# Performance work log

Measured on AMD Instinct MI355X. Metric: run time of the kernel, lower is better.

The kernel has to match this reference:

```python
import jax, jax.numpy as jnp
import numpy as np
from jax import lax

NPOINT = 1024
RADIUS = 0.4
NSAMPLE = 32


def _fps(xyz, m):
    """Farthest point sampling. xyz: (B,N,3) -> idx (B,m) int32."""
    B, N, _ = xyz.shape
    init_idx = jnp.zeros((B,), jnp.int32)

    def step(carry, _):
        dists, last = carry  # dists (B,N), last (B,)
        last_pt = jnp.take_along_axis(xyz, last[:, None, None], axis=1)  # (B,1,3)
        d = jnp.sum((xyz - last_pt) ** 2, axis=-1)  # (B,N)
        dists = jnp.minimum(dists, d)
        nxt = jnp.argmax(dists, axis=-1).astype(jnp.int32)
        return (dists, nxt), nxt

    (_, _), rest = lax.scan(step, (jnp.full((B, N), 1e10, jnp.float32), init_idx),
                            None, length=m - 1)
    return jnp.concatenate([init_idx[None, :], rest], axis=0).T  # (B,m)


def _ball_query(xyz, new_xyz, radius, k):
    """First-k in-radius neighbors (CUDA ball_query semantics: pad with first hit).
    xyz (B,N,3), new_xyz (B,M,3) -> (B,M,k) int32."""
    N = xyz.shape[1]
    d2 = jnp.sum((new_xyz[:, :, None, :] - xyz[:, None, :, :]) ** 2, axis=-1)  # (B,M,N)
    idx = jnp.where(d2 < radius * radius, jnp.arange(N, dtype=jnp.int32), jnp.int32(N))
    neg_topk, _ = lax.top_k(-idx, k)        # k smallest indices
    idx_k = -neg_topk                        # (B,M,k), invalid == N
    valid = idx_k < N
    first = idx_k[..., :1]                   # first (closest-index) hit
    return jnp.where(valid, idx_k, first)


def _gather(pts, idx):
    """pts (B,N,D), idx (B,M,K) -> (B,M,K,D)."""
    return jax.vmap(lambda p, i: p[i])(pts, idx)


def setup_inputs() -> dict:
    key = jax.random.key(0)
    ks = jax.random.split(key, 6)
    B, N, C = 8, 8192, 64
    cin = C + 3
    xyz = jax.random.normal(ks[0], (B, N, 3), jnp.float32)
    features = jax.random.normal(ks[1], (B, N, C), jnp.float32)
    w1 = jax.random.normal(ks[2], (64, cin), jnp.float32) * 0.05
    b1 = jnp.zeros((64,), jnp.float32)
    w2 = jax.random.normal(ks[3], (64, 64), jnp.float32) * 0.05
    b2 = jnp.zeros((64,), jnp.float32)
    w3 = jax.random.normal(ks[4], (128, 64), jnp.float32) * 0.05
    b3 = jnp.zeros((128,), jnp.float32)
    return {"xyz": xyz, "features": features, "w1": w1, "b1": b1,
            "w2": w2, "b2": b2, "w3": w3, "b3": b3}


def reference(xyz, features, w1, b1, w2, b2, w3, b3):
    # FPS sample npoint centers (pool=True branch)
    fps_idx = _fps(xyz, NPOINT)                                   # (B,M)
    new_xyz = jnp.take_along_axis(xyz, fps_idx[..., None], axis=1)  # (B,M,3)
    # ball-query grouping with use_xyz=True (relative coords prepended)
    gidx = _ball_query(xyz, new_xyz, RADIUS, NSAMPLE)             # (B,M,K)
    gxyz = _gather(xyz, gidx) - new_xyz[:, :, None, :]            # (B,M,K,3)
    gfeat = _gather(features, gidx)                               # (B,M,K,C)
    x = jnp.concatenate([gxyz, gfeat], axis=-1)                   # (B,M,K,3+C)
    # shared MLP (1x1 convs) + ReLU
    h = jax.nn.relu(jnp.einsum('bmkc,oc->bmko', x, w1) + b1)
    h = jax.nn.relu(jnp.einsum('bmkc,oc->bmko', h, w2) + b2)
    h = jax.nn.relu(jnp.einsum('bmkc,oc->bmko', h, w3) + b3)      # (B,M,K,128)
    # max-pool over group dim -> (B, C_out, M) like torch (B, mlp[-1], npoint)
    new_features = jnp.transpose(jnp.max(h, axis=2), (0, 2, 1))
    return new_xyz, new_features
```

## Files before the change

### kernel.cpp

```cpp
#include <hip/hip_runtime.h>
#include <stdint.h>

#define BB 8
#define NN 8192
#define NPOINT 1024
#define NSAMPLE 32
#define XS 104
#define HS 72

typedef short short8 __attribute__((ext_vector_type(8)));
typedef float floatx4 __attribute__((ext_vector_type(4)));
typedef float f32x2 __attribute__((ext_vector_type(2)));

__device__ __forceinline__ unsigned short f2bf(float f) {
    unsigned u = __float_as_uint(f);
    unsigned r = u + 0x7FFFu + ((u >> 16) & 1u);
    return (unsigned short)(r >> 16);
}

__device__ __forceinline__ unsigned long long u64max(unsigned long long a,
                                                     unsigned long long b) {
    return (a > b) ? a : b;
}

template <int CTRL, int RMASK>
__device__ __forceinline__ unsigned long long dpp_max_step(unsigned long long key) {
    int lo = (int)(unsigned int)(key & 0xffffffffull);
    int hi = (int)(unsigned int)(key >> 32);
    int tlo = __builtin_amdgcn_update_dpp(0, lo, CTRL, RMASK, 0xF, true);
    int thi = __builtin_amdgcn_update_dpp(0, hi, CTRL, RMASK, 0xF, true);
    unsigned long long t = ((unsigned long long)(unsigned int)thi << 32) |
                           (unsigned long long)(unsigned int)tlo;
    return u64max(key, t);
}

__device__ __forceinline__ unsigned long long dpp_wave_max(unsigned long long key) {
    key = dpp_max_step<0x111, 0xF>(key);
    key = dpp_max_step<0x112, 0xF>(key);
    key = dpp_max_step<0x114, 0xF>(key);
    key = dpp_max_step<0x118, 0xF>(key);
    key = dpp_max_step<0x142, 0xA>(key);
    key = dpp_max_step<0x143, 0xC>(key);
    return key;
}

__device__ __forceinline__ void fps_bar() {
    asm volatile("s_waitcnt lgkmcnt(0)" ::: "memory");
    __builtin_amdgcn_s_barrier();
    asm volatile("" ::: "memory");
}

__global__ __launch_bounds__(256) void mega_kernel(
    const float* __restrict__ xyz, const float* __restrict__ features,
    const float* __restrict__ w1, const float* __restrict__ b1,
    const float* __restrict__ w2, const float* __restrict__ b2,
    const float* __restrict__ w3, const float* __restrict__ b3,
    float* __restrict__ new_xyz, float* __restrict__ out_feat,
    unsigned* __restrict__ sel) {
    __shared__ __align__(16) char smem[98432];

    const int t = threadIdx.x;
    const int lane = t & 63;

    if (blockIdx.x < BB) {
#pragma clang fp contract(off)
        const int b = blockIdx.x;
        float* sxyz = (float*)smem;
        unsigned long long* wred = (unsigned long long*)(smem + 98304);
        const int wv = t >> 6;
        const float* base = xyz + (size_t)b * NN * 3;
        unsigned* selb = sel + b * NPOINT;

        f32x2 px2[16], py2[16], pz2[16];
        float dist[32];
#pragma unroll
        for (int i = 0; i < 32; ++i) {
            int p = t + (i << 8);
            float x = base[p * 3 + 0];
            float y = base[p * 3 + 1];
            float z = base[p * 3 + 2];
            sxyz[p * 3 + 0] = x; sxyz[p * 3 + 1] = y; sxyz[p * 3 + 2] = z;
            if (i & 1) { px2[i >> 1].y = x; py2[i >> 1].y = y; pz2[i >> 1].y = z; }
            else       { px2[i >> 1].x = x; py2[i >> 1].x = y; pz2[i >> 1].x = z; }
            dist[i] = 1e10f;
        }
        __syncthreads();

        float lx = sxyz[0], ly = sxyz[1], lz = sxyz[2];
        float* outb = new_xyz + (size_t)b * NPOINT * 3;
        if (t == 0) {
            outb[0] = lx; outb[1] = ly; outb[2] = lz;
            __hip_atomic_store(&selb[0], 1u, __ATOMIC_RELAXED,
                               __HIP_MEMORY_SCOPE_AGENT);
        }

        for (int j = 1; j < NPOINT; ++j) {
            float bd0 = -1.0f, bd1 = -1.0f;
            int bi0 = 0, bi1 = 16;
            f32x2 lx2; lx2.x = lx; lx2.y = lx;
            f32x2 ly2; ly2.x = ly; ly2.y = ly;
            f32x2 lz2; lz2.x = lz; lz2.y = lz;
#pragma unroll
            for (int jj = 0; jj < 16; ++jj) {
                f32x2 dx = px2[jj] - lx2;
                f32x2 dy = py2[jj] - ly2;
                f32x2 dz = pz2[jj] - lz2;
                f32x2 xx = dx * dx;
                f32x2 yy = dy * dy;
                f32x2 zz = dz * dz;
                f32x2 s1 = xx + yy;
                f32x2 d2 = s1 + zz;
                float d0 = fminf(dist[2 * jj], d2.x);
                dist[2 * jj] = d0;
                float d1 = fminf(dist[2 * jj + 1], d2.y);
                dist[2 * jj + 1] = d1;
                bool ge = d0 >= d1;
                float pm = ge ? d0 : d1;
                int pi = ge ? (2 * jj) : (2 * jj + 1);
                if (jj < 8) {
                    bool gt = pm > bd0;
                    bd0 = gt ? pm : bd0;
                    bi0 = gt ? pi : bi0;
                } else {
                    bool gt = pm > bd1;
                    bd1 = gt ? pm : bd1;
                    bi1 = gt ? pi : bi1;
                }
            }
            unsigned long long key0 =
                ((unsigned long long)__float_as_uint(bd0) << 32) |
                (unsigned long long)(~(unsigned int)(t + (bi0 << 8)));
            unsigned long long key1 =
                ((unsigned long long)__float_as_uint(bd1) << 32) |
                (unsigned long long)(~(unsigned int)(t + (bi1 << 8)));
            unsigned long long key = u64max(key0, key1);
            key = dpp_wave_max(key);
            if (lane == 63) wred[(j & 1) * 4 + wv] = key;
            fps_bar();
            int cur;
            {
                const unsigned long long* wr = &wred[(j & 1) * 4];
                ulonglong2 p01 = *(const ulonglong2*)&wr[0];
                ulonglong2 p23 = *(const ulonglong2*)&wr[2];
                unsigned long long m = u64max(u64max(p01.x, p01.y),
                                              u64max(p23.x, p23.y));
                cur = (int)(~(unsigned int)(m & 0xffffffffull));
            }
            {
                const float* cp = &sxyz[cur * 3];
                float3 c = *(const float3*)cp;
                lx = c.x; ly = c.y; lz = c.z;
            }
            if (t == 0) {
                outb[j * 3 + 0] = lx;
                outb[j * 3 + 1] = ly;
                outb[j * 3 + 2] = lz;
                __hip_atomic_store(&selb[j], (unsigned)(cur + 1),
                                   __ATOMIC_RELAXED, __HIP_MEMORY_SCOPE_AGENT);
            }
        }
    } else {
        const int i = blockIdx.x - BB;
        const int b = i & 7;
        const int g = i >> 3;
        unsigned short* s_x = (unsigned short*)smem;
        unsigned short* s_h = (unsigned short*)(smem + 26624);
        unsigned short* s_w12 = (unsigned short*)(smem + 45056);
        int* s_gi = (int*)(smem + 67584);
        int* s_sel4 = (int*)(smem + 68096);

        const int w = t >> 6;
        const int col = lane & 15;
        const int quad = lane >> 4;

        {
            int o = t >> 2, part = t & 3;
            const float* w1r = w1 + o * 67;
#pragma unroll
            for (int ii = 0; ii < 26; ++ii) {
                int c = part * 26 + ii;
                float v = 0.0f;
                if (c < 64) v = w1r[3 + c];
                else if (c < 67) v = w1r[c - 64];
                s_w12[o * XS + c] = f2bf(v);
            }
            const float* w2r = w2 + o * 64 + part * 16;
#pragma unroll
            for (int ii = 0; ii < 8; ++ii) {
                unsigned pk = (unsigned)f2bf(w2r[2 * ii]) |
                              ((unsigned)f2bf(w2r[2 * ii + 1]) << 16);
                *(unsigned*)&s_w12[6656 + o * HS + part * 16 + 2 * ii] = pk;
            }
        }

        if (t < 4) {
            unsigned* sp = sel + b * NPOINT + (g << 2) + t;
            unsigned v;
            while ((( v = __hip_atomic_load(sp, __ATOMIC_RELAXED,
                                            __HIP_MEMORY_SCOPE_AGENT)) - 1u) > 8191u)
                __builtin_amdgcn_s_sleep(32);
            s_sel4[t] = (int)(v - 1u);
        }
        __syncthreads();

        {
            const int cidx = s_sel4[w];
            const float* base = xyz + (size_t)b * NN * 3;
            const float cx = base[cidx * 3 + 0];
            const float cy = base[cidx * 3 + 1];
            const float cz = base[cidx * 3 + 2];
            const float R2 = (float)(0.4 * 0.4);

            int have = 0;
            for (int chunk = 0; chunk < (NN / 64) && have < NSAMPLE; ++chunk) {
                int p = (chunk << 6) + lane;
                float dx = __fsub_rn(cx, base[p * 3 + 0]);
                float dy = __fsub_rn(cy, base[p * 3 + 1]);
                float dz = __fsub_rn(cz, base[p * 3 + 2]);
                float d2 = __fadd_rn(__fadd_rn(__fmul_rn(dx, dx), __fmul_rn(dy, dy)),
                                     __fmul_rn(dz, dz));
                bool in = d2 < R2;
                unsigned long long m = __ballot(in);
                int pre = __popcll(m & ((1ull << lane) - 1ull));
                int slot = have + pre;
                if (in && slot < NSAMPLE) s_gi[w * NSAMPLE + slot] = p;
                have += (int)__popcll(m);
            }
            if (lane < NSAMPLE) {
                int first = s_gi[w * NSAMPLE];
                int v = (lane < have) ? s_gi[w * NSAMPLE + lane] : first;
                s_gi[w * NSAMPLE + lane] = v;
            }
        }
        __syncthreads();

        {
            int k = t >> 1, half = t & 1;
            int row = s_gi[k];
            const float4* frow =
                (const float4*)(features + ((size_t)b * NN + row) * 64) + half * 8;
            unsigned short* xr = &s_x[k * XS + half * 32];
#pragma unroll
            for (int ii = 0; ii < 8; ++ii) {
                float4 v = frow[ii];
                unsigned lo = (unsigned)f2bf(v.x) | ((unsigned)f2bf(v.y) << 16);
                unsigned hi = (unsigned)f2bf(v.z) | ((unsigned)f2bf(v.w) << 16);
                *(uint2*)(xr + ii * 4) = make_uint2(lo, hi);
            }
        }
        if (t < 128) {
            int k = t;
            int row = s_gi[k];
            int cidx = s_sel4[k >> 5];
            const float* pr = xyz + ((size_t)b * NN + row) * 3;
            const float* cr = xyz + ((size_t)b * NN + cidx) * 3;
            s_x[k * XS + 64] = f2bf(pr[0] - cr[0]);
            s_x[k * XS + 65] = f2bf(pr[1] - cr[1]);
            s_x[k * XS + 66] = f2bf(pr[2] - cr[2]);
            s_x[k * XS + 67] = 0;
            unsigned* z = (unsigned*)&s_x[k * XS + 68];
#pragma unroll
            for (int ii = 0; ii < 14; ++ii) z[ii] = 0;
        }
        __syncthreads();

        const int mbase = w * 32;

        floatx4 acc[2][4] = {};
        for (int kk = 0; kk < 3; ++kk) {
            short8 a0 = *(const short8*)&s_x[(mbase + col) * XS + kk * 32 + quad * 8];
            short8 a1 = *(const short8*)&s_x[(mbase + 16 + col) * XS + kk * 32 + quad * 8];
#pragma unroll
            for (int nt = 0; nt < 4; ++nt) {
                short8 bfr = *(const short8*)&s_w12[(nt * 16 + col) * XS + kk * 32 + quad * 8];
                acc[0][nt] = __builtin_amdgcn_mfma_f32_16x16x32_bf16(a0, bfr, acc[0][nt], 0, 0, 0);
                acc[1][nt] = __builtin_amdgcn_mfma_f32_16x16x32_bf16(a1, bfr, acc[1][nt], 0, 0, 0);
            }
        }
#pragma unroll
        for (int nt = 0; nt < 4; ++nt) {
            float bb = b1[nt * 16 + col];
#pragma unroll
            for (int mt = 0; mt < 2; ++mt)
#pragma unroll
                for (int r = 0; r < 4; ++r) {
                    float v = fmaxf(acc[mt][nt][r] + bb, 0.0f);
                    s_h[(mbase + mt * 16 + quad * 4 + r) * HS + nt * 16 + col] = f2bf(v);
                }
        }
        __syncthreads();

        floatx4 acc2[2][4] = {};
        for (int kk = 0; kk < 2; ++kk) {
            short8 a0 = *(const short8*)&s_h[(mbase + col) * HS + kk * 32 + quad * 8];
            short8 a1 = *(const short8*)&s_h[(mbase + 16 + col) * HS + kk * 32 + quad * 8];
#pragma unroll
            for (int nt = 0; nt < 4; ++nt) {
                short8 bfr = *(const short8*)&s_w12[6656 + (nt * 16 + col) * HS + kk * 32 + quad * 8];
                acc2[0][nt] = __builtin_amdgcn_mfma_f32_16x16x32_bf16(a0, bfr, acc2[0][nt], 0, 0, 0);
                acc2[1][nt] = __builtin_amdgcn_mfma_f32_16x16x32_bf16(a1, bfr, acc2[1][nt], 0, 0, 0);
            }
        }
        unsigned short* s_h2 = s_x;
#pragma unroll
        for (int nt = 0; nt < 4; ++nt) {
            float bb = b2[nt * 16 + col];
#pragma unroll
            for (int mt = 0; mt < 2; ++mt)
#pragma unroll
                for (int r = 0; r < 4; ++r) {
                    float v = fmaxf(acc2[mt][nt][r] + bb, 0.0f);
                    s_h2[(mbase + mt * 16 + quad * 4 + r) * HS + nt * 16 + col] = f2bf(v);
                }
        }
        __syncthreads();

        {
            int o = t >> 1, half = t & 1;
            const float* w3r = w3 + o * 64 + half * 32;
#pragma unroll
            for (int ii = 0; ii < 16; ++ii) {
                unsigned pk = (unsigned)f2bf(w3r[2 * ii]) |
                              ((unsigned)f2bf(w3r[2 * ii + 1]) << 16);
                *(unsigned*)&s_w12[o * HS + half * 32 + 2 * ii] = pk;
            }
        }
        __syncthreads();

        floatx4 c3[2][8] = {};
        for (int kk = 0; kk < 2; ++kk) {
            short8 a0 = *(const short8*)&s_h2[(mbase + col) * HS + kk * 32 + quad * 8];
            short8 a1 = *(const short8*)&s_h2[(mbase + 16 + col) * HS + kk * 32 + quad * 8];
#pragma unroll
            for (int nt = 0; nt < 8; ++nt) {
                short8 bfr = *(const short8*)&s_w12[(nt * 16 + col) * HS + kk * 32 + quad * 8];
                c3[0][nt] = __builtin_amdgcn_mfma_f32_16x16x32_bf16(a0, bfr, c3[0][nt], 0, 0, 0);
                c3[1][nt] = __builtin_amdgcn_mfma_f32_16x16x32_bf16(a1, bfr, c3[1][nt], 0, 0, 0);
            }
        }
        {
            int gg = (g << 2) + w;
            float* ob = out_feat + (size_t)b * (128 * 1024) + gg;
#pragma unroll
            for (int nt = 0; nt < 8; ++nt) {
                float m = fmaxf(fmaxf(fmaxf(c3[0][nt][0], c3[0][nt][1]),
                                      fmaxf(c3[0][nt][2], c3[0][nt][3])),
                                fmaxf(fmaxf(c3[1][nt][0], c3[1][nt][1]),
                                      fmaxf(c3[1][nt][2], c3[1][nt][3])));
                m = fmaxf(m, __shfl_xor(m, 16));
                m = fmaxf(m, __shfl_xor(m, 32));
                if (lane < 16) {
                    float v = fmaxf(m + b3[nt * 16 + lane], 0.0f);
                    ob[(size_t)(nt * 16 + lane) * 1024] = v;
                }
            }
        }
    }
}

extern "C" void kernel_launch(void* const* d_in, const int* in_sizes, int n_in,
                              void* d_out, int out_size, void* d_ws, size_t ws_size,
                              hipStream_t stream) {
    const float* xyz      = (const float*)d_in[0];
    const float* features = (const float*)d_in[1];
    const float* w1       = (const float*)d_in[2];
    const float* b1       = (const float*)d_in[3];
    const float* w2       = (const float*)d_in[4];
    const float* b2       = (const float*)d_in[5];
    const float* w3       = (const float*)d_in[6];
    const float* b3       = (const float*)d_in[7];

    float* out      = (float*)d_out;
    float* new_xyz  = out;
    float* out_feat = out + BB * NPOINT * 3;
    unsigned* sel   = (unsigned*)d_ws;

    mega_kernel<<<BB + (BB * NPOINT) / 4, 256, 0, stream>>>(
        xyz, features, w1, b1, w2, b2, w3, b3, new_xyz, out_feat, sel);
}
```

Before: 1.009 ms.

## Replace FPS workgroup barrier with LDS flag-polling handshake per iteration

The per-iteration block barrier in farthest-point sampling is removed. Each wave's final lane now writes its argmax key together with the iteration number and an XOR checksum into double-buffered LDS slots. All waves spin on the four slots until every one carries the current iteration and a valid checksum. This is meant to cut barrier latency on the serial 1023-step critical path, but it relies on LDS write visibility and ordering without a fence, and the spin loop may cost cycles or risk reading torn data.

```diff
diff --git a/kernel.cpp b/kernel.cpp
--- a/kernel.cpp
+++ b/kernel.cpp
@@ -44,12 +44,6 @@
     return key;
 }
 
-__device__ __forceinline__ void fps_bar() {
-    asm volatile("s_waitcnt lgkmcnt(0)" ::: "memory");
-    __builtin_amdgcn_s_barrier();
-    asm volatile("" ::: "memory");
-}
-
 __global__ __launch_bounds__(256) void mega_kernel(
     const float* __restrict__ xyz, const float* __restrict__ features,
     const float* __restrict__ w1, const float* __restrict__ b1,
@@ -66,7 +60,7 @@
 #pragma clang fp contract(off)
         const int b = blockIdx.x;
         float* sxyz = (float*)smem;
-        unsigned long long* wred = (unsigned long long*)(smem + 98304);
+        uint4* wred4 = (uint4*)(smem + 98304);
         const int wv = t >> 6;
         const float* base = xyz + (size_t)b * NN * 3;
         unsigned* selb = sel + b * NPOINT;
@@ -84,6 +78,7 @@
             else       { px2[i >> 1].x = x; py2[i >> 1].x = y; pz2[i >> 1].x = z; }
             dist[i] = 1e10f;
         }
+        if (t < 8) wred4[t] = make_uint4(0u, 0u, 0u, 1u);
         __syncthreads();
 
         float lx = sxyz[0], ly = sxyz[1], lz = sxyz[2];
@@ -135,15 +130,38 @@
                 (unsigned long long)(~(unsigned int)(t + (bi1 << 8)));
             unsigned long long key = u64max(key0, key1);
             key = dpp_wave_max(key);
-            if (lane == 63) wred[(j & 1) * 4 + wv] = key;
-            fps_bar();
+
+            if (lane == 63) {
+                unsigned lo = (unsigned)(key & 0xffffffffull);
+                unsigned hi = (unsigned)(key >> 32);
+                uint4 e;
+                e.x = lo; e.y = hi; e.z = (unsigned)j;
+                e.w = lo ^ hi ^ (unsigned)j;
+                wred4[((j & 1) << 2) + wv] = e;
+            }
+            asm volatile("" ::: "memory");
+
             int cur;
             {
-                const unsigned long long* wr = &wred[(j & 1) * 4];
-                ulonglong2 p01 = *(const ulonglong2*)&wr[0];
-                ulonglong2 p23 = *(const ulonglong2*)&wr[2];
-                unsigned long long m = u64max(u64max(p01.x, p01.y),
-                                              u64max(p23.x, p23.y));
+                const uint4* wb = &wred4[(j & 1) << 2];
+                uint4 e0, e1, e2, e3;
+                const unsigned jt = (unsigned)j;
+                for (;;) {
+                    asm volatile("" ::: "memory");
+                    e0 = wb[0]; e1 = wb[1]; e2 = wb[2]; e3 = wb[3];
+                    bool ok = (e0.z == jt) & (e1.z == jt) &
+                              (e2.z == jt) & (e3.z == jt) &
+                              (e0.w == (e0.x ^ e0.y ^ e0.z)) &
+                              (e1.w == (e1.x ^ e1.y ^ e1.z)) &
+                              (e2.w == (e2.x ^ e2.y ^ e2.z)) &
+                              (e3.w == (e3.x ^ e3.y ^ e3.z));
+                    if (ok) break;
+                }
+                unsigned long long k0 = ((unsigned long long)e0.y << 32) | e0.x;
+                unsigned long long k1 = ((unsigned long long)e1.y << 32) | e1.x;
+                unsigned long long k2 = ((unsigned long long)e2.y << 32) | e2.x;
+                unsigned long long k3 = ((unsigned long long)e3.y << 32) | e3.x;
+                unsigned long long m = u64max(u64max(k0, k1), u64max(k2, k3));
                 cur = (int)(~(unsigned int)(m & 0xffffffffull));
             }
             {
```

Result: slower. 1.122 ms (+11.2%).
